# Kernel optimization log

Measured on AMD Instinct MI355X. Metric: run time of the kernel, lower is better.

The kernel has to match this reference:

```python
import jax, jax.numpy as jnp
import numpy as np
import math

B, T, C, NH, LEVEL = 2, 2048, 1024, 16, 3


def _build_sets(T, level):
    # hierarchical dyadic sets: levels `level`..floor(log2(T)), step 2^l
    sets = []
    levelmax = int(math.floor(math.log2(T)))
    for l in range(level, levelmax + 1):
        step = 2 ** l
        for i in range(T // step):
            sets.append((i * step, (i + 1) * step - 1))
    b = np.asarray(sets, dtype=np.int32)
    return b[:, 0], b[:, 1]


def setup_inputs() -> dict:
    key = jax.random.key(0)
    kx, kw1, kw2 = jax.random.split(key, 3)
    x = jax.random.normal(kx, (B, T, C), dtype=jnp.float32)
    # torch nn.Linear stores weight as (out_features, in_features); y = x @ W.T
    W_attn = jax.random.normal(kw1, (3 * C, C), dtype=jnp.float32) * (C ** -0.5)
    W_proj = jax.random.normal(kw2, (C, C), dtype=jnp.float32) * (C ** -0.5)
    return {"x": x, "W_attn": W_attn, "W_proj": W_proj}


def _get_slice(xc, l_idx, r_idx):
    # xc: (B,NH,T,hs) cumulative sums; returns sum over [l_idx, r_idx]
    r = xc[:, :, r_idx, :]
    l = xc[:, :, l_idx - 1, :] * (l_idx >= 1)[None, None, :, None].astype(xc.dtype)
    return r - l


def _forward(x, W_attn, W_proj):
    hs = C // NH
    scale = hs ** -0.5
    qkv = x @ W_attn.T                      # (B,T,3C)
    q, k, v = jnp.split(qkv, 3, axis=2)
    heads = lambda t: t.reshape(B, T, NH, hs).transpose(0, 2, 1, 3)  # (B,NH,T,hs)
    q, k, v = heads(q), heads(k), heads(v)
    phi = lambda t: jax.nn.elu(t) + 1.0     # feature_map = 'elu_plus'
    q_phi, k_phi = phi(q), phi(k)
    k_cum = jnp.cumsum(k_phi, axis=2)
    v_cum = jnp.cumsum(v, axis=2)

    l_np, r_np = _build_sets(T, LEVEL)
    l_idx, r_idx = jnp.asarray(l_np), jnp.asarray(r_np)
    K = _get_slice(k_cum, l_idx, r_idx)     # (B,NH,S,hs)
    V = _get_slice(v_cum, l_idx, r_idx)

    t_idx = jnp.arange(T)
    mask = t_idx[:, None] >= r_idx[None, :]                 # (T,S)
    logits = jnp.einsum('bhtd,bhsd->bhts', q, K) * scale    # raw q here (as in source)
    logits = jnp.where(mask[None, None], logits, -jnp.inf)

    # tail term over last (t mod 2^level)+1 tokens, uses q_phi
    Lmin = 2 ** LEVEL
    tail_len = t_idx % Lmin + 1
    l_tail = t_idx - tail_len + 1
    K_tail = _get_slice(k_cum, l_tail, t_idx)               # (B,NH,T,hs)
    V_tail = _get_slice(v_cum, l_tail, t_idx)
    tail_logit = jnp.sum(q_phi * K_tail, axis=-1) * scale   # (B,NH,T)

    full = jnp.concatenate([logits, tail_logit[..., None]], axis=-1)
    att = jax.nn.softmax(full, axis=-1)
    out = jnp.einsum('bhts,bhsd->bhtd', att[..., :-1], V) + att[..., -1:] * V_tail
    out = out.transpose(0, 2, 1, 3).reshape(B, T, C)
    return out @ W_proj.T


def reference(x, W_attn, W_proj):
    return _forward(x, W_attn, W_proj)
```

## Files before the change

kernel.cpp:

```cpp
#include <hip/hip_runtime.h>
#include <hip/hip_bf16.h>
#include <stdint.h>

#define B_    2
#define T_    2048
#define CD    1024
#define NH_   16
#define HS_   64
#define NSETS 511
#define NSP   512
#define QKV_LD 3072
#define NEGBIG (-3.4e38f)
#define QSC   (0.125f * 1.44269504088896f)

typedef __attribute__((ext_vector_type(8))) short  short8;
typedef __attribute__((ext_vector_type(4))) float  f32x4;
typedef _Float16 half8v __attribute__((ext_vector_type(8)));

__device__ __forceinline__ unsigned short f2bf(float f) {
  unsigned u = __float_as_uint(f);
  unsigned r = 0x7FFFu + ((u >> 16) & 1u);
  return (unsigned short)((u + r) >> 16);
}
__device__ __forceinline__ float bf2f(unsigned short h) {
  return __uint_as_float(((unsigned)h) << 16);
}
__device__ __forceinline__ unsigned short f2h(float v) {
  _Float16 h = (_Float16)v;
  return __builtin_bit_cast(unsigned short, h);
}
__device__ __forceinline__ float elu1(float x) {
  return x > 0.f ? x + 1.f : __expf(x);
}
__device__ __forceinline__ void gload16(const unsigned short* g, short* l) {
  __builtin_amdgcn_global_load_lds(
      (const __attribute__((address_space(1))) unsigned int*)g,
      (__attribute__((address_space(3))) unsigned int*)l, 16, 0, 0);
}

__global__ __launch_bounds__(256) void split3_kernel(
    const float* __restrict__ x, const float* __restrict__ Wa,
    const float* __restrict__ Wp,
    unsigned short* __restrict__ xh, unsigned short* __restrict__ xl,
    unsigned short* __restrict__ xf,
    unsigned short* __restrict__ waqh, unsigned short* __restrict__ waql,
    unsigned short* __restrict__ wakvf, unsigned short* __restrict__ wph) {
  int bid = blockIdx.x;
  int t = threadIdx.x;
  if (bid < 16384) {
    int i = bid * 256 + t;
    float v = x[i];
    unsigned short h = f2bf(v);
    xh[i] = h;
    xl[i] = f2bf(v - bf2f(h));
    xf[i] = f2h(v);
  } else if (bid < 20480) {
    int i = (bid - 16384) * 256 + t;
    float v = Wa[i];
    unsigned short h = f2bf(v);
    waqh[i] = h;
    waql[i] = f2bf(v - bf2f(h));
  } else if (bid < 28672) {
    int i = (bid - 20480) * 256 + t;
    wakvf[i] = f2h(Wa[1048576 + i]);
  } else {
    int i = (bid - 28672) * 256 + t;
    wph[i] = f2bf(Wp[i]);
  }
}

template<int SPLIT, int BN, int F16>
__device__ __forceinline__ void gemm_body(
    short* lds,
    const unsigned short* __restrict__ Ah, const unsigned short* __restrict__ Al,
    const unsigned short* __restrict__ Bh, const unsigned short* __restrict__ Bl,
    float* __restrict__ Cmat, int K, int ldc, int row0, int col0)
{
  constexpr int NB   = BN / 16;
  constexpr int ALD  = 8 * (1 + SPLIT);
  constexpr int TL   = ALD + NB * (1 + SPLIT);
  constexpr int PW   = TL / 4;
  constexpr int ASH  = (1 + SPLIT) * 4096;
  constexpr int ABYT = ASH * 2;
  constexpr int NC   = BN / 32;

  const int tid  = threadIdx.x;
  const int lane = tid & 63;
  const int w    = tid >> 6;
  const int wr   = w >> 1, wc = w & 1;

  f32x4 acc[4][NC];
  #pragma unroll
  for (int a = 0; a < 4; ++a)
    #pragma unroll
    for (int b = 0; b < NC; ++b)
      acc[a][b] = (f32x4){0.f, 0.f, 0.f, 0.f};

  const int rlane = lane & 15;
  const int kgrp  = lane >> 4;
  const int rsw   = (kgrp ^ (rlane & 3) ^ ((rlane >> 2) & 3)) << 4;

  const int slr = lane >> 2;
  const int sch = (lane & 3) ^ (slr & 3) ^ ((slr >> 2) & 3);

  for (int kt = 0; kt < K; kt += 32) {
    __syncthreads();
    #pragma unroll
    for (int li = 0; li < PW; ++li) {
      int L = w * PW + li;
      const unsigned short* src; int dsts; size_t rowb;
      if (L < 8)                { src = Ah; rowb = (size_t)row0 + L * 16;       dsts = L * 512; }
      else if (SPLIT && L < 16) { src = Al; rowb = (size_t)row0 + (L - 8) * 16; dsts = 4096 + (L - 8) * 512; }
      else {
        int Lb = L - ALD;
        if (!SPLIT || Lb < NB) { src = Bh; rowb = (size_t)col0 + Lb * 16;        dsts = ASH + Lb * 512; }
        else                   { src = Bl; rowb = (size_t)col0 + (Lb - NB) * 16; dsts = ASH + BN * 32 + (Lb - NB) * 512; }
      }
      gload16(src + (rowb + slr) * K + kt + (sch << 3), lds + dsts + lane * 8);
    }
    __syncthreads();

    short8 aH[4], bH[NC], aL[4], bL[NC];
    #pragma unroll
    for (int m = 0; m < 4; ++m) {
      int r = wr * 64 + m * 16 + rlane;
      aH[m] = *(const short8*)((const char*)lds + r * 64 + rsw);
      if (SPLIT) aL[m] = *(const short8*)((const char*)lds + 8192 + r * 64 + rsw);
    }
    #pragma unroll
    for (int n = 0; n < NC; ++n) {
      int c = wc * (BN / 2) + n * 16 + rlane;
      bH[n] = *(const short8*)((const char*)lds + ABYT + c * 64 + rsw);
      if (SPLIT) bL[n] = *(const short8*)((const char*)lds + ABYT + BN * 64 + c * 64 + rsw);
    }
    #pragma unroll
    for (int mm = 0; mm < 4; ++mm)
      #pragma unroll
      for (int nn = 0; nn < NC; ++nn) {
        if (F16) {
          acc[mm][nn] = __builtin_amdgcn_mfma_f32_16x16x32_f16(
              __builtin_bit_cast(half8v, aH[mm]), __builtin_bit_cast(half8v, bH[nn]),
              acc[mm][nn], 0, 0, 0);
        } else {
          acc[mm][nn] = __builtin_amdgcn_mfma_f32_16x16x32_bf16(aH[mm], bH[nn], acc[mm][nn], 0, 0, 0);
          if (SPLIT) {
            acc[mm][nn] = __builtin_amdgcn_mfma_f32_16x16x32_bf16(aH[mm], bL[nn], acc[mm][nn], 0, 0, 0);
            acc[mm][nn] = __builtin_amdgcn_mfma_f32_16x16x32_bf16(aL[mm], bH[nn], acc[mm][nn], 0, 0, 0);
          }
        }
      }
  }

  const int rl = (lane >> 4) * 4;
  const int cl = lane & 15;
  #pragma unroll
  for (int mm = 0; mm < 4; ++mm)
    #pragma unroll
    for (int nn = 0; nn < NC; ++nn)
      #pragma unroll
      for (int r = 0; r < 4; ++r) {
        int row = row0 + wr * 64 + mm * 16 + rl + r;
        int col = col0 + wc * (BN / 2) + nn * 16 + cl;
        Cmat[(size_t)row * ldc + col] = acc[mm][nn][r];
      }
}

template<int SPLIT, int BN, int F16>
__global__ __launch_bounds__(256) void gemm_bt(
    const unsigned short* __restrict__ Ah, const unsigned short* __restrict__ Al,
    const unsigned short* __restrict__ Bh, const unsigned short* __restrict__ Bl,
    float* __restrict__ Cmat, int M, int N, int K, int ldc)
{
  __shared__ short lds[(1 + SPLIT) * 4096 + (1 + SPLIT) * BN * 32];
  const int nwg = gridDim.x;
  const int cpx = nwg >> 3;
  const int bid = blockIdx.x;
  const int swb = (bid & 7) * cpx + (bid >> 3);
  const int nbx = N / BN;
  const int bx = swb % nbx;
  const int by = swb / nbx;
  gemm_body<SPLIT, BN, F16>(lds, Ah, Al, Bh, Bl, Cmat, K, ldc, by * 128, bx * BN);
}

__global__ __launch_bounds__(256) void cs_part(const float* __restrict__ qkv,
                                               float* __restrict__ part) {
  int blk = blockIdx.x;
  int q   = blk & 1;
  int seg = (blk >> 1) & 127;
  int b   = blk >> 8;
  int c   = threadIdx.x * 4;
  const float* src = qkv + (size_t)(b * T_ + seg * 16) * QKV_LD + CD + q * CD + c;
  float4 s = {0.f, 0.f, 0.f, 0.f};
  #pragma unroll 4
  for (int j = 0; j < 16; ++j) {
    float4 v = *(const float4*)(src + (size_t)j * QKV_LD);
    if (q == 0) {
      s.x += elu1(v.x); s.y += elu1(v.y); s.z += elu1(v.z); s.w += elu1(v.w);
    } else {
      s.x += v.x; s.y += v.y; s.z += v.z; s.w += v.w;
    }
  }
  *(float4*)(part + ((size_t)(b * 128 + seg) * 2048) + q * 1024 + c) = s;
}

__global__ __launch_bounds__(256) void cs_final(const float* __restrict__ qkv,
                                                const float* __restrict__ part,
                                                float* __restrict__ kcum,
                                                float* __restrict__ vcum) {
  int blk = blockIdx.x;
  int q   = blk & 1;
  int seg = (blk >> 1) & 127;
  int b   = blk >> 8;
  int c   = threadIdx.x * 4;
  int h   = c >> 6, d = c & 63;
  float4 s = {0.f, 0.f, 0.f, 0.f};
  const float* pb = part + (size_t)(b * 128) * 2048 + q * 1024 + c;
  #pragma unroll 8
  for (int ss = 0; ss < seg; ++ss) {
    float4 p = *(const float4*)(pb + (size_t)ss * 2048);
    s.x += p.x; s.y += p.y; s.z += p.z; s.w += p.w;
  }
  const float* src = qkv + (size_t)(b * T_ + seg * 16) * QKV_LD + CD + q * CD + c;
  float* dst = (q == 0 ? kcum : vcum) + ((size_t)(b * NH_ + h) * T_ + seg * 16) * HS_ + d;
  #pragma unroll 4
  for (int j = 0; j < 16; ++j) {
    float4 v = *(const float4*)(src + (size_t)j * QKV_LD);
    if (q == 0) {
      s.x += elu1(v.x); s.y += elu1(v.y); s.z += elu1(v.z); s.w += elu1(v.w);
    } else {
      s.x += v.x; s.y += v.y; s.z += v.z; s.w += v.w;
    }
    *(float4*)(dst + (size_t)j * HS_) = s;
  }
}

__global__ __launch_bounds__(256) void build_sets2(
    const float* __restrict__ kcum, const float* __restrict__ vcum,
    unsigned short* __restrict__ Ksh, unsigned short* __restrict__ Ksl,
    unsigned short* __restrict__ Vst, int* __restrict__ r_srt)
{
  __shared__ int   lr[64], lli[64];
  __shared__ float vt[64][65];
  const int bh = blockIdx.x >> 3;
  const int s0 = (blockIdx.x & 7) * 64;
  const int tid = threadIdx.x;

  for (int s = tid; s < NSP; s += 256) {
    int r, li, rank;
    if (s == NSETS) { r = 0x7fffffff; li = 0; rank = NSETS; }
    else {
      int lvl = 3, base = 0;
      while (s >= base + (T_ >> lvl)) { base += T_ >> lvl; ++lvl; }
      int i = s - base;
      int m = (i + 1) << lvl;
      r = m - 1; li = i << lvl;
      rank = lvl - 3;
      #pragma unroll
      for (int j = 3; j <= 11; ++j) rank += (m - 8) >> j;
    }
    if (rank >= s0 && rank < s0 + 64) {
      lr[rank - s0]  = r;
      lli[rank - s0] = li;
      if (bh == 0) r_srt[rank] = r;
    }
  }
  __syncthreads();

  const int sl = tid >> 2;
  const int dq = (tid & 3) * 16;
  const int r  = lr[sl], li = lli[sl];
  const size_t orow = ((size_t)(bh << 9) + s0 + sl) * HS_ + dq;
  short8 kh0, kh1, kl0, kl1;
  if (r == 0x7fffffff) {
    #pragma unroll
    for (int j = 0; j < 8; ++j) { kh0[j]=0; kh1[j]=0; kl0[j]=0; kl1[j]=0; }
    #pragma unroll
    for (int j = 0; j < 16; ++j) vt[sl][dq + j] = 0.f;
  } else {
    const float* kr0 = kcum + ((size_t)bh * T_ + r) * HS_ + dq;
    const float* vr0 = vcum + ((size_t)bh * T_ + r) * HS_ + dq;
    const float* kr1 = kcum + ((size_t)bh * T_ + (li - 1)) * HS_ + dq;
    const float* vr1 = vcum + ((size_t)bh * T_ + (li - 1)) * HS_ + dq;
    #pragma unroll
    for (int g = 0; g < 4; ++g) {
      float4 kv = *(const float4*)(kr0 + g * 4);
      float4 vv = *(const float4*)(vr0 + g * 4);
      if (li > 0) {
        float4 k1 = *(const float4*)(kr1 + g * 4);
        float4 v1 = *(const float4*)(vr1 + g * 4);
        kv.x -= k1.x; kv.y -= k1.y; kv.z -= k1.z; kv.w -= k1.w;
        vv.x -= v1.x; vv.y -= v1.y; vv.z -= v1.z; vv.w -= v1.w;
      }
      float ka[4] = {kv.x, kv.y, kv.z, kv.w};
      float va[4] = {vv.x, vv.y, vv.z, vv.w};
      #pragma unroll
      for (int j = 0; j < 4; ++j) {
        int e = g * 4 + j;
        unsigned short h = f2bf(ka[j]);
        unsigned short l = f2bf(ka[j] - bf2f(h));
        if (e < 8) { kh0[e] = (short)h; kl0[e] = (short)l; }
        else       { kh1[e - 8] = (short)h; kl1[e - 8] = (short)l; }
        vt[sl][dq + e] = va[j];
      }
    }
  }
  *(short8*)(Ksh + orow)     = kh0;
  *(short8*)(Ksh + orow + 8) = kh1;
  *(short8*)(Ksl + orow)     = kl0;
  *(short8*)(Ksl + orow + 8) = kl1;
  __syncthreads();

  const int d  = tid >> 2;
  const int sq = (tid & 3) * 16;
  short8 a, b2;
  #pragma unroll
  for (int j = 0; j < 8; ++j) {
    a[j]  = (short)f2bf(vt[sq + j][d]);
    b2[j] = (short)f2bf(vt[sq + 8 + j][d]);
  }
  unsigned short* dst = Vst + ((size_t)(bh << 6) + d) * NSP + s0 + sq;
  *(short8*)dst = a;
  *(short8*)(dst + 8) = b2;
}

__global__ __launch_bounds__(256) void attn_mfma(
    const float* __restrict__ qkv, const float* __restrict__ kcum,
    const float* __restrict__ vcum,
    const unsigned short* __restrict__ Ksh, const unsigned short* __restrict__ Ksl,
    const unsigned short* __restrict__ Vst, const int* __restrict__ r_srt,
    unsigned short* __restrict__ attnb)
{
  __shared__ __align__(16) short Pl[4 * 1024];
  __shared__ __align__(16) short KV[3 * 4096];
  __shared__ int rs_lds[NSP];

  const int blk = blockIdx.x;
  const int xcd = blk & 7;
  const int j   = blk >> 3;
  const int bh  = xcd * 4 + (j >> 5);
  const int tch = (j + ((j >> 5) << 3)) & 31;
  const int b = bh >> 4, h = bh & 15;
  const int t0 = tch * 64;
  const int tid = threadIdx.x;
  const int lane = tid & 63;
  const int w = tid >> 6;
  const int col = lane & 15;
  const int kgrp = (lane >> 4) * 8;

  const int srow = lane >> 3;
  const int scsw = ((lane & 7) ^ srow) * 8;

  int nmax = 0;
  #pragma unroll
  for (int jj = 3; jj <= 11; ++jj) nmax += (t0 + 64) >> jj;
  const int ntiles = (nmax + 63) >> 6;

  const unsigned short* srcp[6];
  int dsts[6], adv[6];
  #pragma unroll
  for (int li = 0; li < 6; ++li) {
    int L = w * 6 + li;
    int a = L >> 3, i = L & 7;
    if (a == 0)      srcp[li] = Ksh + ((size_t)(bh << 9) + i * 8 + srow) * 64 + scsw;
    else if (a == 1) srcp[li] = Ksl + ((size_t)(bh << 9) + i * 8 + srow) * 64 + scsw;
    else             srcp[li] = Vst + ((size_t)(bh << 6) + i * 8 + srow) * NSP + scsw;
    dsts[li] = (a * 4096 + i * 512 + lane * 8) * 2;
    adv[li]  = (a < 2) ? 4096 : 64;
  }
  float4 stg[6];
  #pragma unroll
  for (int li = 0; li < 6; ++li) stg[li] = *(const float4*)srcp[li];

  short8 qh[2], ql[2];
  {
    int qrow = t0 + w * 16 + col;
    const float* qr = qkv + (size_t)(b * T_ + qrow) * QKV_LD + h * HS_;
    #pragma unroll
    for (int ks = 0; ks < 2; ++ks) {
      float4 v0 = *(const float4*)(qr + kgrp + ks * 32);
      float4 v1 = *(const float4*)(qr + kgrp + ks * 32 + 4);
      float vv[8] = {v0.x, v0.y, v0.z, v0.w, v1.x, v1.y, v1.z, v1.w};
      #pragma unroll
      for (int jj = 0; jj < 8; ++jj) {
        float sv = vv[jj] * QSC;
        unsigned short hi = f2bf(sv);
        qh[ks][jj] = (short)hi;
        ql[ks][jj] = (short)f2bf(sv - bf2f(hi));
      }
    }
  }
  for (int s = tid; s < NSP; s += 256) rs_lds[s] = r_srt[s];

  int rows[4];
  #pragma unroll
  for (int r = 0; r < 4; ++r) rows[r] = t0 + w * 16 + (lane >> 4) * 4 + r;

  f32x4 O[4];
  float mrun[4], lsum[4];
  #pragma unroll
  for (int f = 0; f < 4; ++f) {
    O[f] = (f32x4){0.f, 0.f, 0.f, 0.f};
    mrun[f] = NEGBIG; lsum[f] = 0.f;
  }

  for (int tile = 0; tile < ntiles; ++tile) {
    const int s0 = tile * 64;
    #pragma unroll
    for (int li = 0; li < 6; ++li)
      *(float4*)((char*)KV + dsts[li]) = stg[li];
    __syncthreads();

    if (tile + 1 < ntiles) {
      #pragma unroll
      for (int li = 0; li < 6; ++li) {
        srcp[li] += adv[li];
        stg[li] = *(const float4*)srcp[li];
      }
    }

    const char* kc = (const char*)KV;
    f32x4 S[4];
    #pragma unroll
    for (int f = 0; f < 4; ++f) S[f] = (f32x4){0.f, 0.f, 0.f, 0.f};

    #pragma unroll
    for (int ks = 0; ks < 2; ++ks) {
      int chnk = (lane >> 4) + ks * 4;
      #pragma unroll
      for (int f = 0; f < 4; ++f) {
        int so = f * 16 + col;
        int kb = so * 128 + ((chnk ^ (so & 7)) << 4);
        short8 bHv = *(const short8*)(kc + kb);
        short8 bLv = *(const short8*)(kc + 8192 + kb);
        S[f] = __builtin_amdgcn_mfma_f32_16x16x32_bf16(qh[ks], bHv, S[f], 0, 0, 0);
        S[f] = __builtin_amdgcn_mfma_f32_16x16x32_bf16(qh[ks], bLv, S[f], 0, 0, 0);
        S[f] = __builtin_amdgcn_mfma_f32_16x16x32_bf16(ql[ks], bHv, S[f], 0, 0, 0);
      }
    }

    int rsv[4];
    #pragma unroll
    for (int f = 0; f < 4; ++f) rsv[f] = rs_lds[s0 + f * 16 + col];

    float zv[4][4];
    #pragma unroll
    for (int f = 0; f < 4; ++f)
      #pragma unroll
      for (int r = 0; r < 4; ++r)
        zv[f][r] = (rsv[f] > rows[r]) ? NEGBIG : S[f][r];

    float mx[4];
    #pragma unroll
    for (int r = 0; r < 4; ++r)
      mx[r] = fmaxf(fmaxf(zv[0][r], zv[1][r]), fmaxf(zv[2][r], zv[3][r]));
    int pred = (mx[0] <= mrun[0] + 11.5f) & (mx[1] <= mrun[1] + 11.5f) &
               (mx[2] <= mrun[2] + 11.5f) & (mx[3] <= mrun[3] + 11.5f);
    if (!__all(pred)) {
      #pragma unroll
      for (int r = 0; r < 4; ++r) {
        float mt = mx[r];
        mt = fmaxf(mt, __shfl_xor(mt, 1));
        mt = fmaxf(mt, __shfl_xor(mt, 2));
        mt = fmaxf(mt, __shfl_xor(mt, 4));
        mt = fmaxf(mt, __shfl_xor(mt, 8));
        float mv = fmaxf(mrun[r], mt);
        float fs = exp2f(mrun[r] - mv);
        lsum[r] *= fs;
        #pragma unroll
        for (int f = 0; f < 4; ++f) O[f][r] *= fs;
        mrun[r] = mv;
      }
    }

    char* pw = (char*)Pl + w * 2048;
    #pragma unroll
    for (int r = 0; r < 4; ++r) {
      int rowr = (lane >> 4) * 4 + r;
      int rswz = (rowr & 7) << 4;
      #pragma unroll
      for (int f = 0; f < 4; ++f) {
        float p = exp2f(zv[f][r] - mrun[r]);
        p = (rsv[f] > rows[r]) ? 0.f : p;
        lsum[r] += p;
        int addr = (rowr * 128 + (f * 16 + col) * 2) ^ rswz;
        *(unsigned short*)(pw + addr) = f2bf(p);
      }
    }

    #pragma unroll
    for (int ks = 0; ks < 2; ++ks) {
      int chnk = (lane >> 4) + ks * 4;
      int pbyte = (col * 128 + (kgrp + ks * 32) * 2) ^ ((col & 7) << 4);
      short8 pa = *(const short8*)(pw + pbyte);
      #pragma unroll
      for (int f = 0; f < 4; ++f) {
        int dr = f * 16 + col;
        short8 bv = *(const short8*)(kc + 16384 + dr * 128 + ((chnk ^ (dr & 7)) << 4));
        O[f] = __builtin_amdgcn_mfma_f32_16x16x32_bf16(pa, bv, O[f], 0, 0, 0);
      }
    }

    __syncthreads();
  }

  float lrun[4];
  #pragma unroll
  for (int r = 0; r < 4; ++r) {
    float l = lsum[r];
    l += __shfl_xor(l, 1);
    l += __shfl_xor(l, 2);
    l += __shfl_xor(l, 4);
    l += __shfl_xor(l, 8);
    lrun[r] = l;
  }

  float ztail;
  {
    int trow = lane >> 2;
    int t = t0 + w * 16 + trow;
    int d0 = (lane & 3) * 16;
    const float* qr = qkv + (size_t)(b * T_ + t) * QKV_LD + h * HS_ + d0;
    float qv[16];
    #pragma unroll
    for (int jj = 0; jj < 4; ++jj) {
      float4 v = *(const float4*)(qr + jj * 4);
      qv[jj*4+0] = v.x; qv[jj*4+1] = v.y; qv[jj*4+2] = v.z; qv[jj*4+3] = v.w;
    }
    int lt = t & ~7;
    const float* kc1 = kcum + ((size_t)bh * T_ + t) * HS_ + d0;
    float kt[16];
    if (lt > 0) {
      const float* kc0 = kcum + ((size_t)bh * T_ + (lt - 1)) * HS_ + d0;
      #pragma unroll
      for (int jj = 0; jj < 16; ++jj) kt[jj] = kc1[jj] - kc0[jj];
    } else {
      #pragma unroll
      for (int jj = 0; jj < 16; ++jj) kt[jj] = kc1[jj];
    }
    float z = 0.f;
    #pragma unroll
    for (int jj = 0; jj < 16; ++jj) {
      float qp = qv[jj] > 0.f ? qv[jj] + 1.f : __expf(qv[jj]);
      z += qp * kt[jj];
    }
    z += __shfl_xor(z, 1);
    z += __shfl_xor(z, 2);
    ztail = z * QSC;
  }

  #pragma unroll
  for (int r = 0; r < 4; ++r) {
    float zt = __shfl(ztail, ((lane >> 4) * 4 + r) * 4);
    float mv = fmaxf(mrun[r], zt);
    float fs = exp2f(mrun[r] - mv);
    float pwgt = exp2f(zt - mv);
    lrun[r] = lrun[r] * fs + pwgt;
    int tr = rows[r];
    int ltr = tr & ~7;
    #pragma unroll
    for (int f = 0; f < 4; ++f) {
      int d = f * 16 + col;
      float v1 = vcum[((size_t)bh * T_ + tr) * HS_ + d];
      float vt = (ltr > 0) ? v1 - vcum[((size_t)bh * T_ + (ltr - 1)) * HS_ + d] : v1;
      O[f][r] = O[f][r] * fs + pwgt * vt;
    }
  }

  #pragma unroll
  for (int r = 0; r < 4; ++r) {
    float inv = 1.f / lrun[r];
    unsigned short* orow = attnb + (size_t)(b * T_ + rows[r]) * CD + h * HS_;
    #pragma unroll
    for (int f = 0; f < 4; ++f)
      orow[f * 16 + col] = f2bf(O[f][r] * inv);
  }
}

extern "C" void kernel_launch(void* const* d_in, const int* in_sizes, int n_in,
                              void* d_out, int out_size, void* d_ws, size_t ws_size,
                              hipStream_t stream) {
  const float* x  = (const float*)d_in[0];
  const float* Wa = (const float*)d_in[1];
  const float* Wp = (const float*)d_in[2];
  float* out = (float*)d_out;

  char* ws = (char*)d_ws;
  size_t off = 0;
  auto alloc = [&](size_t bytes) -> char* {
    char* p = ws + off;
    off += (bytes + 255) & ~(size_t)255;
    return p;
  };

  const int M = B_ * T_;
  float* qkv  = (float*)alloc((size_t)M * QKV_LD * 4);
  float* kcum = (float*)alloc((size_t)B_ * NH_ * T_ * HS_ * 4);
  float* vcum = (float*)alloc((size_t)B_ * NH_ * T_ * HS_ * 4);
  float* part = (float*)alloc((size_t)B_ * 128 * 2048 * 4);
  unsigned short* wph = (unsigned short*)alloc((size_t)CD * CD * 2);

  unsigned short* xf    = (unsigned short*)kcum;
  unsigned short* wakvf = (unsigned short*)vcum;

  char* regionA = alloc((size_t)16777216);
  unsigned short* xh = (unsigned short*)regionA;
  unsigned short* xl = (unsigned short*)(regionA + (size_t)M * CD * 2);
  const size_t SETS_ELEMS = (size_t)B_ * NH_ * NSP * HS_;
  unsigned short* Ksh = (unsigned short*)regionA;
  unsigned short* Ksl = Ksh + SETS_ELEMS;
  unsigned short* Vst = (unsigned short*)(regionA + 2 * SETS_ELEMS * 2);
  int*            r_srt = (int*)(regionA + 3 * SETS_ELEMS * 2);

  char* regionB = alloc((size_t)12582912);
  unsigned short* waqh = (unsigned short*)regionB;
  unsigned short* waql = (unsigned short*)(regionB + (size_t)CD * CD * 2);
  unsigned short* attnb = (unsigned short*)regionB;

  split3_kernel<<<dim3(32768), dim3(256), 0, stream>>>(
      x, Wa, Wp, xh, xl, xf, waqh, waql, wakvf, wph);

  gemm_bt<1, 64, 0><<<dim3(512), dim3(256), 0, stream>>>(
      xh, xl, waqh, waql, qkv, M, 1024, CD, QKV_LD);

  gemm_bt<0, 128, 1><<<dim3(512), dim3(256), 0, stream>>>(
      xf, (const unsigned short*)nullptr, wakvf, (const unsigned short*)nullptr,
      qkv + 1024, M, 2048, CD, QKV_LD);

  cs_part<<<dim3(B_ * 128 * 2), dim3(256), 0, stream>>>(qkv, part);
  cs_final<<<dim3(B_ * 128 * 2), dim3(256), 0, stream>>>(qkv, part, kcum, vcum);

  build_sets2<<<dim3(B_ * NH_ * 8), dim3(256), 0, stream>>>(
      kcum, vcum, Ksh, Ksl, Vst, r_srt);

  attn_mfma<<<dim3(1024), dim3(256), 0, stream>>>(
      qkv, kcum, vcum, Ksh, Ksl, Vst, r_srt, attnb);

  gemm_bt<0, 64, 0><<<dim3(512), dim3(256), 0, stream>>>(
      attnb, (const unsigned short*)nullptr, wph, (const unsigned short*)nullptr,
      out, M, 1024, CD, CD);
}
```

Before: 204.6 us.

## Stage K/V tiles with direct global-to-LDS loads instead of register prefetch

The attention kernel used to prefetch the next K-high, K-low and V tile into registers during the current tile's compute, then write them to LDS. It now issues per-tile 16-byte global-to-LDS loads through a `gload16` helper, with addresses recomputed from the tile offset, right before the barrier. This removes the six float4 staging registers per thread and the extra register-to-LDS store pass, which may ease register pressure. In exchange, tile loads no longer overlap the previous tile's MFMA work, and correctness depends on `gload16` completing before `__syncthreads`. The LDS arrays also lose their explicit 16-byte alignment.

```diff
diff --git a/kernel.cpp b/kernel.cpp
--- a/kernel.cpp
+++ b/kernel.cpp
@@ -330,9 +330,9 @@
     const unsigned short* __restrict__ Vst, const int* __restrict__ r_srt,
     unsigned short* __restrict__ attnb)
 {
-  __shared__ __align__(16) short Pl[4 * 1024];
-  __shared__ __align__(16) short KV[3 * 4096];
-  __shared__ int rs_lds[NSP];
+  __shared__ short Pl[4 * 1024];
+  __shared__ short KV[3 * 4096];
+  __shared__ int   rs_lds[NSP];
 
   const int blk = blockIdx.x;
   const int xcd = blk & 7;
@@ -350,26 +350,17 @@
   const int srow = lane >> 3;
   const int scsw = ((lane & 7) ^ srow) * 8;
 
-  int nmax = 0;
-  #pragma unroll
-  for (int jj = 3; jj <= 11; ++jj) nmax += (t0 + 64) >> jj;
-  const int ntiles = (nmax + 63) >> 6;
-
-  const unsigned short* srcp[6];
-  int dsts[6], adv[6];
-  #pragma unroll
-  for (int li = 0; li < 6; ++li) {
-    int L = w * 6 + li;
-    int a = L >> 3, i = L & 7;
-    if (a == 0)      srcp[li] = Ksh + ((size_t)(bh << 9) + i * 8 + srow) * 64 + scsw;
-    else if (a == 1) srcp[li] = Ksl + ((size_t)(bh << 9) + i * 8 + srow) * 64 + scsw;
-    else             srcp[li] = Vst + ((size_t)(bh << 6) + i * 8 + srow) * NSP + scsw;
-    dsts[li] = (a * 4096 + i * 512 + lane * 8) * 2;
-    adv[li]  = (a < 2) ? 4096 : 64;
-  }
-  float4 stg[6];
-  #pragma unroll
-  for (int li = 0; li < 6; ++li) stg[li] = *(const float4*)srcp[li];
+  auto stage_tile = [&](int s0) {
+    #pragma unroll
+    for (int L = w * 6; L < w * 6 + 6; ++L) {
+      int a = L >> 3, i = L & 7;
+      const unsigned short* src;
+      if (a == 0)      src = Ksh + ((size_t)(bh << 9) + s0 + i * 8 + srow) * 64 + scsw;
+      else if (a == 1) src = Ksl + ((size_t)(bh << 9) + s0 + i * 8 + srow) * 64 + scsw;
+      else             src = Vst + ((size_t)(bh << 6) + i * 8 + srow) * NSP + s0 + scsw;
+      gload16(src, KV + a * 4096 + i * 512 + lane * 8);
+    }
+  };
 
   short8 qh[2], ql[2];
   {
@@ -403,20 +394,15 @@
     mrun[f] = NEGBIG; lsum[f] = 0.f;
   }
 
+  int nmax = 0;
+  #pragma unroll
+  for (int jj = 3; jj <= 11; ++jj) nmax += (t0 + 64) >> jj;
+  const int ntiles = (nmax + 63) >> 6;
+
   for (int tile = 0; tile < ntiles; ++tile) {
     const int s0 = tile * 64;
-    #pragma unroll
-    for (int li = 0; li < 6; ++li)
-      *(float4*)((char*)KV + dsts[li]) = stg[li];
+    stage_tile(s0);
     __syncthreads();
-
-    if (tile + 1 < ntiles) {
-      #pragma unroll
-      for (int li = 0; li < 6; ++li) {
-        srcp[li] += adv[li];
-        stg[li] = *(const float4*)srcp[li];
-      }
-    }
 
     const char* kc = (const char*)KV;
     f32x4 S[4];
```

After: 185.9 us. 9.2% less time.
